# Kernel optimization log

Hardware: AMD Instinct MI355X
Metric: run time of the kernel (lower is better)

## Reference

```python
import jax, jax.numpy as jnp
import numpy as np

HEADS, DK, DV, STRIDE = 8, 32, 32, 2
EPS = 1e-5

def dwconv(x, w, b, stride):
    # depthwise 3x3, padding 1; w: [C,1,3,3]
    y = jax.lax.conv_general_dilated(
        x, w, (stride, stride), ((1, 1), (1, 1)),
        dimension_numbers=("NCHW", "OIHW", "NCHW"),
        feature_group_count=x.shape[1])
    return y + b[None, :, None, None]

def setup_inputs() -> dict:
    key = jax.random.key(0)
    ks = jax.random.split(key, 16)
    B_, C, H, W = 8, 256, 56, 56
    hd = HEADS * DK
    s = lambda k, shp: (jax.random.normal(k, shp, jnp.float32) * 0.02)
    return {
        "x": jax.random.normal(ks[0], (B_, C, H, W), jnp.float32),
        "Wk_dw": s(ks[1], (C, 1, 3, 3)), "bk_dw": jnp.zeros((C,), jnp.float32),
        "Wv_dw": s(ks[2], (C, 1, 3, 3)), "bv_dw": jnp.zeros((C,), jnp.float32),
        "Wq": s(ks[3], (hd, C)), "bq": jnp.zeros((hd,), jnp.float32),
        "Wk": s(ks[4], (hd, C)), "bk": jnp.zeros((hd,), jnp.float32),
        "Wv": s(ks[5], (HEADS * DV, C)), "bv": jnp.zeros((HEADS * DV,), jnp.float32),
        "Wo": s(ks[6], (C, HEADS * DV)), "bo": jnp.zeros((C,), jnp.float32),
        "Bbias": s(ks[7], (1, HEADS, H * W, (H // STRIDE) * (W // STRIDE))),
    }

def reference(x, Wk_dw, bk_dw, Wv_dw, bv_dw, Wq, bq, Wk, bk, Wv, bv, Wo, bo, Bbias):
    b, c, h, w = x.shape
    xr = x.reshape(b, c, h * w).transpose(0, 2, 1)  # [b, hw, c]
    # F.layer_norm with normalized_shape=(b, hw, c): single mean/var over ALL elements
    mu = jnp.mean(xr)
    var = jnp.mean((xr - mu) ** 2)
    xn = (xr - mu) * jax.lax.rsqrt(var + EPS)
    q = (xn @ Wq.T + bq).reshape(b, h * w, HEADS, DK).transpose(0, 2, 1, 3)  # [b,H,hw,dk]
    ki = dwconv(x, Wk_dw, bk_dw, STRIDE)
    kh, kw = ki.shape[2], ki.shape[3]
    kf = ki.reshape(b, c, kh * kw).transpose(0, 2, 1)
    k = (kf @ Wk.T + bk).reshape(b, kh * kw, HEADS, DK).transpose(0, 2, 1, 3)
    vi = dwconv(x, Wv_dw, bv_dw, STRIDE)
    vf = vi.reshape(b, c, kh * kw).transpose(0, 2, 1)
    v = (vf @ Wv.T + bv).reshape(b, kh * kw, HEADS, DV).transpose(0, 2, 1, 3)
    attn = jnp.einsum("bhid,bhjd->bhij", q, k) * (DK ** -0.5) + Bbias
    attn = jax.nn.softmax(attn, axis=-1)
    res = jnp.einsum("bhij,bhjd->bhid", attn, v).transpose(0, 2, 1, 3)
    res = res.reshape(b, h * w, HEADS * DV)
    out = (res @ Wo.T + bo).reshape(b, c, h, w)  # faithful to original .view (no transpose)
    return out + x
```

## Files before the change

### kernel.cpp

```cpp
#include <hip/hip_runtime.h>

typedef unsigned short u16;
typedef unsigned int   u32;
typedef __attribute__((ext_vector_type(8))) short short8;
typedef __attribute__((ext_vector_type(4))) float f32x4;
typedef __attribute__((ext_vector_type(4))) unsigned short us4;

#define MFMA16(a, b, c) __builtin_amdgcn_mfma_f32_16x16x32_bf16((a), (b), (c), 0, 0, 0)

static constexpr int B_ = 8;
static constexpr int HW = 3136;
static constexpr int KW = 784;
static constexpr int NELEM = B_ * 256 * HW;
static constexpr int NBB = 8 * HW * KW;

static constexpr size_t OFF_CNT = 4096;
static constexpr size_t OFF_W   = 8192;
static constexpr int AOFF_WQ = 0, AOFF_WK = 65536, AOFF_WV = 131072, AOFF_WO = 196608;
static constexpr int AOFF_WKDW = 262144, AOFF_WVDW = 264448;
static constexpr int AOFF_BKDW = 266752, AOFF_BVDW = 267008, AOFF_BQ = 267264;
static constexpr int AOFF_BK = 267520, AOFF_BV = 267776, AOFF_BO = 268032;
static constexpr size_t OFF_XT  = 557056;
static constexpr size_t SZ_XT   = (size_t)B_ * HW * 256 * 2;
static constexpr size_t SZ_KJ   = (size_t)B_ * KW * 256 * 2;
static constexpr size_t OFF_KIT = OFF_XT + SZ_XT;
static constexpr size_t OFF_VIT = OFF_KIT + SZ_KJ;
static constexpr size_t OFF_KI  = OFF_VIT + SZ_KJ;
static constexpr size_t OFF_VI  = OFF_KI + SZ_KJ;
static constexpr size_t OFF_Q   = OFF_VI + SZ_KJ;
static constexpr size_t OFF_O   = OFF_XT;
static constexpr size_t OFF_BB  = OFF_Q + SZ_XT;
static constexpr size_t SZ_BB   = (size_t)NBB * 2;

__device__ __forceinline__ float bf2f(u16 u) { return __uint_as_float(((u32)u) << 16); }
__device__ __forceinline__ u16 f2bf(float f) {
  u32 u = __float_as_uint(f);
  u32 r = u + 0x7FFFu + ((u >> 16) & 1u);
  return (u16)(r >> 16);
}
__device__ __forceinline__ u32 cvtpk(float lo, float hi) {
  u32 r;
  asm("v_cvt_pk_bf16_f32 %0, %1, %2" : "=v"(r) : "v"(lo), "v"(hi));
  return r;
}

__global__ __launch_bounds__(256) void detect_k(const u32* __restrict__ x, int* __restrict__ cnt) {
  int c = 0;
  for (int i = threadIdx.x; i < 4096; i += 256) {
    float v = __uint_as_float(x[i] << 16);
    if (fabsf(v) > 1e4f) c++;
  }
#pragma unroll
  for (int off = 32; off > 0; off >>= 1) c += __shfl_down(c, off);
  if ((threadIdx.x & 63) == 0) atomicAdd(cnt, c);
}

struct CvtArgs { const void* src[12]; int dstoff[12]; int n[12]; };
__global__ __launch_bounds__(256) void cvtw_k(CvtArgs a, u16* __restrict__ arena,
                                              const int* __restrict__ cnt) {
  int t = blockIdx.y;
  int n = a.n[t];
  u16* d = arena + a.dstoff[t];
  int f32m = (*cnt >= 64);
  if (f32m) {
    const float* s = (const float*)a.src[t];
    for (int i = blockIdx.x * 256 + threadIdx.x; i < n; i += gridDim.x * 256) d[i] = f2bf(s[i]);
  } else {
    const u16* s = (const u16*)a.src[t];
    for (int i = blockIdx.x * 256 + threadIdx.x; i < n; i += gridDim.x * 256) d[i] = s[i];
  }
}

__global__ __launch_bounds__(256) void cvtb_k(const void* __restrict__ src, u16* __restrict__ dst,
                                              const int* __restrict__ cnt) {
  int f32m = (*cnt >= 64);
  const int n4 = NBB / 4;
  if (f32m) {
    const float4* s = (const float4*)src;
    us4* d = (us4*)dst;
    for (int i = blockIdx.x * 256 + threadIdx.x; i < n4; i += gridDim.x * 256) {
      float4 v = s[i];
      us4 o = {f2bf(v.x), f2bf(v.y), f2bf(v.z), f2bf(v.w)};
      d[i] = o;
    }
  } else {
    const uint2* s = (const uint2*)src;
    uint2* d = (uint2*)dst;
    for (int i = blockIdx.x * 256 + threadIdx.x; i < n4; i += gridDim.x * 256) d[i] = s[i];
  }
}

__global__ __launch_bounds__(256) void reduce_k(const void* __restrict__ x, double* __restrict__ acc,
                                                const int* __restrict__ cnt) {
  int f32m = (*cnt >= 64);
  float s = 0.f, ss = 0.f;
  if (f32m) {
    const float4* xv = (const float4*)x;
    const int n4 = NELEM / 4;
    for (int i = blockIdx.x * 256 + threadIdx.x; i < n4; i += gridDim.x * 256) {
      float4 u = xv[i];
      s += u.x + u.y + u.z + u.w;
      ss += u.x * u.x + u.y * u.y + u.z * u.z + u.w * u.w;
    }
  } else {
    const uint4* xv = (const uint4*)x;
    const int n8 = NELEM / 8;
    for (int i = blockIdx.x * 256 + threadIdx.x; i < n8; i += gridDim.x * 256) {
      uint4 u = xv[i];
      u32 w[4] = {u.x, u.y, u.z, u.w};
#pragma unroll
      for (int q = 0; q < 4; q++) {
        float f0 = __uint_as_float(w[q] << 16);
        float f1 = __uint_as_float(w[q] & 0xFFFF0000u);
        s += f0 + f1;
        ss += f0 * f0 + f1 * f1;
      }
    }
  }
#pragma unroll
  for (int off = 32; off > 0; off >>= 1) {
    s += __shfl_down(s, off);
    ss += __shfl_down(ss, off);
  }
  __shared__ float as_[4], ass_[4];
  int wv = threadIdx.x >> 6;
  if ((threadIdx.x & 63) == 0) { as_[wv] = s; ass_[wv] = ss; }
  __syncthreads();
  if (threadIdx.x == 0) {
    atomicAdd(acc + 0, (double)(as_[0] + as_[1] + as_[2] + as_[3]));
    atomicAdd(acc + 1, (double)(ass_[0] + ass_[1] + ass_[2] + ass_[3]));
  }
}

__global__ __launch_bounds__(256) void prep_k(const u16* __restrict__ wq, const u16* __restrict__ bq,
                                              float* __restrict__ wsf) {
  const double* acc = (const double*)wsf;
  __shared__ float sh[2];
  if (threadIdx.x == 0) {
    double N = (double)NELEM;
    double mu = acc[0] / N;
    double var = acc[1] / N - mu * mu;
    float rstd = (float)(1.0 / sqrt(var + 1e-5));
    sh[0] = (float)mu; sh[1] = rstd;
    wsf[4] = (float)mu; wsf[5] = rstd;
    wsf[6] = rstd * 0.17677669529663687f;
  }
  __syncthreads();
  int o = threadIdx.x;
  float wsum = 0.f;
  for (int c = 0; c < 256; c++) wsum += bf2f(wq[o * 256 + c]);
  wsf[16 + o] = (bf2f(bq[o]) - sh[1] * sh[0] * wsum) * 0.17677669529663687f;
}

__global__ __launch_bounds__(256) void transpose_x_k(const void* __restrict__ src, u16* __restrict__ dst,
                                                     const int* __restrict__ cnt) {
  int f32m = (*cnt >= 64);
  __shared__ u16 t[32][33];
  int b = blockIdx.z;
  int r0 = blockIdx.y * 32, c0 = blockIdx.x * 32;
  int tid = threadIdx.x, col = tid & 31;
  size_t base = (size_t)b * 256 * HW;
  if (f32m) {
    const float* s = (const float*)src + base;
#pragma unroll
    for (int i = 0; i < 4; i++) {
      int row = (tid >> 5) + i * 8;
      t[row][col] = f2bf(s[(size_t)(r0 + row) * HW + c0 + col]);
    }
  } else {
    const u16* s = (const u16*)src + base;
#pragma unroll
    for (int i = 0; i < 4; i++) {
      int row = (tid >> 5) + i * 8;
      t[row][col] = s[(size_t)(r0 + row) * HW + c0 + col];
    }
  }
  __syncthreads();
  u16* d = dst + base;
#pragma unroll
  for (int i = 0; i < 4; i++) {
    int row = (tid >> 5) + i * 8;
    d[(size_t)(c0 + row) * 256 + r0 + col] = t[col][row];
  }
}

__global__ __launch_bounds__(256) void transpose_k(const u16* __restrict__ src, u16* __restrict__ dst,
                                                   int R, int Cc) {
  __shared__ u16 t[32][33];
  int b = blockIdx.z;
  int r0 = blockIdx.y * 32, c0 = blockIdx.x * 32;
  const u16* s = src + (size_t)b * R * Cc;
  u16* d = dst + (size_t)b * R * Cc;
  int tid = threadIdx.x, col = tid & 31;
#pragma unroll
  for (int i = 0; i < 4; i++) {
    int row = (tid >> 5) + i * 8;
    if (r0 + row < R && c0 + col < Cc) t[row][col] = s[(size_t)(r0 + row) * Cc + c0 + col];
  }
  __syncthreads();
#pragma unroll
  for (int i = 0; i < 4; i++) {
    int row = (tid >> 5) + i * 8;
    if (c0 + row < Cc && r0 + col < R) d[(size_t)(c0 + row) * R + r0 + col] = t[col][row];
  }
}

__global__ __launch_bounds__(256) void dwconv_k(const void* __restrict__ x,
                                                const u16* __restrict__ arena,
                                                u16* __restrict__ ki, u16* __restrict__ vi,
                                                const int* __restrict__ cnt) {
  int f32m = (*cnt >= 64);
  int b = blockIdx.x >> 8;
  int c = blockIdx.x & 255;
  float wkf[9], wvf[9];
#pragma unroll
  for (int t = 0; t < 9; t++) {
    wkf[t] = bf2f(arena[AOFF_WKDW + c * 9 + t]);
    wvf[t] = bf2f(arena[AOFF_WVDW + c * 9 + t]);
  }
  float kb = bf2f(arena[AOFF_BKDW + c]), vb = bf2f(arena[AOFF_BVDW + c]);
  size_t xbase = (size_t)(b * 256 + c) * HW;
  auto body = [&](auto LDX) {
    for (int j = threadIdx.x; j < KW; j += 256) {
      int oi = j / 28, oj = j % 28;
      float ka = kb, va = vb;
#pragma unroll
      for (int di = 0; di < 3; di++) {
        int ii = 2 * oi - 1 + di;
        if ((unsigned)ii >= 56u) continue;
#pragma unroll
        for (int dj = 0; dj < 3; dj++) {
          int ij = 2 * oj - 1 + dj;
          if ((unsigned)ij >= 56u) continue;
          float xv = LDX(ii * 56 + ij);
          ka += xv * wkf[di * 3 + dj];
          va += xv * wvf[di * 3 + dj];
        }
      }
      ki[(size_t)(b * 256 + c) * KW + j] = f2bf(ka);
      vi[(size_t)(b * 256 + c) * KW + j] = f2bf(va);
    }
  };
  if (f32m) {
    const float* xp = (const float*)x + xbase;
    body([&](int i) { return xp[i]; });
  } else {
    const u16* xp = (const u16*)x + xbase;
    body([&](int i) { return bf2f(xp[i]); });
  }
}

__global__ __launch_bounds__(256) void proj_q_k(const u16* __restrict__ xt, const u16* __restrict__ Wq,
                                                const float* __restrict__ wsf, u16* __restrict__ q) {
  int lane = threadIdx.x & 63, wave = threadIdx.x >> 6;
  int l15 = lane & 15, quad = lane >> 4;
  int b = blockIdx.x / 49, pb = blockIdx.x % 49;
  int p0 = pb * 64 + wave * 16;
  const u16* arow = xt + ((size_t)(b * HW) + p0 + l15) * 256 + quad * 8;
  short8 af[8];
#pragma unroll
  for (int ks = 0; ks < 8; ks++) af[ks] = *(const short8*)(arow + ks * 32);
  float alpha = wsf[6];
  const float* beta = wsf + 16;
  for (int ot = 0; ot < 16; ot++) {
    const u16* brow = Wq + (size_t)(ot * 16 + l15) * 256 + quad * 8;
    f32x4 acc = {0.f, 0.f, 0.f, 0.f};
#pragma unroll
    for (int ks = 0; ks < 8; ks++) acc = MFMA16(af[ks], *(const short8*)(brow + ks * 32), acc);
    int o = ot * 16 + l15;
    float bet = beta[o];
    size_t base = ((size_t)(b * HW) + p0 + quad * 4) * 256 + o;
#pragma unroll
    for (int r = 0; r < 4; r++) q[base + (size_t)r * 256] = f2bf(alpha * acc[r] + bet);
  }
}

__global__ __launch_bounds__(256) void proj_k_k(const u16* __restrict__ kit, const u16* __restrict__ Wk,
                                                const u16* __restrict__ bk, u16* __restrict__ kout) {
  int lane = threadIdx.x & 63, wave = threadIdx.x >> 6;
  int l15 = lane & 15, quad = lane >> 4;
  int b = blockIdx.x / 13, jb = blockIdx.x % 13;
  int p0 = jb * 64 + wave * 16;
  if (p0 >= KW) return;
  const u16* arow = kit + ((size_t)(b * KW) + p0 + l15) * 256 + quad * 8;
  short8 af[8];
#pragma unroll
  for (int ks = 0; ks < 8; ks++) af[ks] = *(const short8*)(arow + ks * 32);
  for (int ot = 0; ot < 16; ot++) {
    const u16* brow = Wk + (size_t)(ot * 16 + l15) * 256 + quad * 8;
    f32x4 acc = {0.f, 0.f, 0.f, 0.f};
#pragma unroll
    for (int ks = 0; ks < 8; ks++) acc = MFMA16(af[ks], *(const short8*)(brow + ks * 32), acc);
    int o = ot * 16 + l15;
    float bias = bf2f(bk[o]);
    size_t base = ((size_t)(b * KW) + p0 + quad * 4) * 256 + o;
#pragma unroll
    for (int r = 0; r < 4; r++) kout[base + (size_t)r * 256] = f2bf(acc[r] + bias);
  }
}

__global__ __launch_bounds__(256) void proj_v_k(const u16* __restrict__ Wv, const u16* __restrict__ vit,
                                                const u16* __restrict__ bv, u16* __restrict__ vT) {
  int lane = threadIdx.x & 63, wave = threadIdx.x >> 6;
  int l15 = lane & 15, quad = lane >> 4;
  int b = blockIdx.x >> 4;
  int ob = (blockIdx.x >> 2) & 3;
  int js = blockIdx.x & 3;
  int o0 = ob * 64 + wave * 16;
  const u16* arow = Wv + (size_t)(o0 + l15) * 256 + quad * 8;
  short8 af[8];
#pragma unroll
  for (int ks = 0; ks < 8; ks++) af[ks] = *(const short8*)(arow + ks * 32);
  int jt0 = js * 13;
  int jt1 = (jt0 + 13 < 49) ? jt0 + 13 : 49;
  for (int jt = jt0; jt < jt1; jt++) {
    const u16* brow = vit + ((size_t)(b * KW) + jt * 16 + l15) * 256 + quad * 8;
    f32x4 acc = {0.f, 0.f, 0.f, 0.f};
#pragma unroll
    for (int ks = 0; ks < 8; ks++) acc = MFMA16(af[ks], *(const short8*)(brow + ks * 32), acc);
#pragma unroll
    for (int r = 0; r < 4; r++) {
      int o = o0 + quad * 4 + r;
      vT[((size_t)(b * 256) + o) * KW + jt * 16 + l15] = f2bf(acc[r] + bf2f(bv[o]));
    }
  }
}

template <typename LD>
__device__ __forceinline__ void attn_body(const u16* __restrict__ qptr, const u16* __restrict__ kptr,
                                          const u16* __restrict__ vptr, u16* __restrict__ Ob,
                                          int b, int h, int p0, LD ldb) {
  int lane = threadIdx.x & 63;
  int l15 = lane & 15, quad = lane >> 4;
  const u16* qp = qptr + ((size_t)(b * HW) + p0 + l15) * 256 + h * 32 + quad * 8;
  short8 qf0 = *(const short8*)qp;
  short8 qf1 = *(const short8*)(qp + 16 * 256);
  const u16* kb = kptr + (size_t)b * KW * 256 + h * 32 + quad * 8;
  const u16* vb = vptr + ((size_t)(b * 256) + h * 32) * KW;
  const f32x4 zz = {0.f, 0.f, 0.f, 0.f};
  f32x4 o00 = zz, o01 = zz, o10 = zz, o11 = zz;
  float ls0 = 0.f, ls1 = 0.f;
  int sl0 = l15 + ((quad & 1) << 5);
  bool hiq = (quad >= 2);

  auto tile = [&](int jt, u32& q00, u32& q01, u32& q10, u32& q11) {
    short8 kf = *(const short8*)(kb + (size_t)(jt * 16 + l15) * 256);
    f32x4 s0 = MFMA16(kf, qf0, zz);
    f32x4 s1 = MFMA16(kf, qf1, zz);
    f32x4 b0 = ldb(0, jt), b1 = ldb(1, jt);
    float e00 = __expf(fminf(s0[0] + b0[0], 30.f));
    float e01 = __expf(fminf(s0[1] + b0[1], 30.f));
    float e02 = __expf(fminf(s0[2] + b0[2], 30.f));
    float e03 = __expf(fminf(s0[3] + b0[3], 30.f));
    float e10 = __expf(fminf(s1[0] + b1[0], 30.f));
    float e11 = __expf(fminf(s1[1] + b1[1], 30.f));
    float e12 = __expf(fminf(s1[2] + b1[2], 30.f));
    float e13 = __expf(fminf(s1[3] + b1[3], 30.f));
    ls0 += (e00 + e01) + (e02 + e03);
    ls1 += (e10 + e11) + (e12 + e13);
    q00 = cvtpk(e00, e01); q01 = cvtpk(e02, e03);
    q10 = cvtpk(e10, e11); q11 = cvtpk(e12, e13);
  };
  auto gather = [&](u32 pa0, u32 pa1, u32 pb0, u32 pb1) -> short8 {
    u32 a0 = (u32)__shfl((int)pa0, sl0);
    u32 a1 = (u32)__shfl((int)pa1, sl0);
    u32 a2 = (u32)__shfl((int)pa0, sl0 + 16);
    u32 a3 = (u32)__shfl((int)pa1, sl0 + 16);
    u32 c0 = (u32)__shfl((int)pb0, sl0);
    u32 c1 = (u32)__shfl((int)pb1, sl0);
    u32 c2 = (u32)__shfl((int)pb0, sl0 + 16);
    u32 c3 = (u32)__shfl((int)pb1, sl0 + 16);
    union { u32 u[4]; short8 s; } w;
    w.u[0] = hiq ? c0 : a0; w.u[1] = hiq ? c1 : a1;
    w.u[2] = hiq ? c2 : a2; w.u[3] = hiq ? c3 : a3;
    return w.s;
  };
  auto pv = [&](int ch, short8 pf0, short8 pf1) {
    int jo = ch * 32 + quad * 8;
    if (jo > 776) jo = 776;
    short8 v0 = *(const short8*)(vb + (size_t)l15 * KW + jo);
    short8 v1 = *(const short8*)(vb + (size_t)(16 + l15) * KW + jo);
    o00 = MFMA16(pf0, v0, o00); o01 = MFMA16(pf0, v1, o01);
    o10 = MFMA16(pf1, v0, o10); o11 = MFMA16(pf1, v1, o11);
  };

#pragma unroll 2
  for (int ch = 0; ch < 24; ch++) {
    u32 a00, a01, a10, a11, b00, b01, b10, b11;
    tile(ch * 2, a00, a01, a10, a11);
    tile(ch * 2 + 1, b00, b01, b10, b11);
    pv(ch, gather(a00, a01, b00, b01), gather(a10, a11, b10, b11));
  }
  {
    u32 a00, a01, a10, a11;
    tile(48, a00, a01, a10, a11);
    pv(24, gather(a00, a01, 0u, 0u), gather(a10, a11, 0u, 0u));
  }
  ls0 += __shfl_xor(ls0, 16); ls0 += __shfl_xor(ls0, 32);
  ls1 += __shfl_xor(ls1, 16); ls1 += __shfl_xor(ls1, 32);
  float inv0 = 1.f / ls0, inv1 = 1.f / ls1;
  size_t ob0 = ((size_t)(b * HW) + p0 + quad * 4) * 256 + h * 32 + l15;
#pragma unroll
  for (int r = 0; r < 4; r++) {
    float ia = __shfl(inv0, quad * 4 + r);
    float ib = __shfl(inv1, quad * 4 + r);
    Ob[ob0 + (size_t)(r * 256)] = f2bf(o00[r] * ia);
    Ob[ob0 + (size_t)(r * 256) + 16] = f2bf(o01[r] * ia);
    Ob[ob0 + (size_t)(16 * 256 + r * 256)] = f2bf(o10[r] * ib);
    Ob[ob0 + (size_t)(16 * 256 + r * 256) + 16] = f2bf(o11[r] * ib);
  }
}

template <int BMODE>
__global__ __launch_bounds__(64) void attn_k(const u16* __restrict__ q, const u16* __restrict__ k,
                                             const u16* __restrict__ vT, const void* __restrict__ Bb,
                                             u16* __restrict__ Ob, const int* __restrict__ cnt) {
  int lane = threadIdx.x & 63;
  int l15 = lane & 15, quad = lane >> 4;
  int pt = blockIdx.x % 98;
  int t = blockIdx.x / 98;
  int h = t & 7, b = t >> 3;
  int p0 = pt * 32;
  size_t bbase = ((size_t)(h * HW) + p0 + l15) * KW + quad * 4;
  if constexpr (BMODE == 0) {
    const u16* bb = (const u16*)Bb;
    attn_body(q, k, vT, Ob, b, h, p0, [&](int sub, int jt) -> f32x4 {
      us4 v = *(const us4*)(bb + bbase + (size_t)(sub * 16) * KW + jt * 16);
      f32x4 r = {bf2f(v[0]), bf2f(v[1]), bf2f(v[2]), bf2f(v[3])};
      return r;
    });
  } else {
    if (*cnt >= 64) {
      const float* bf = (const float*)Bb;
      attn_body(q, k, vT, Ob, b, h, p0, [&](int sub, int jt) -> f32x4 {
        float4 v = *(const float4*)(bf + bbase + (size_t)(sub * 16) * KW + jt * 16);
        f32x4 r = {v.x, v.y, v.z, v.w};
        return r;
      });
    } else {
      const u16* bb = (const u16*)Bb;
      attn_body(q, k, vT, Ob, b, h, p0, [&](int sub, int jt) -> f32x4 {
        us4 v = *(const us4*)(bb + bbase + (size_t)(sub * 16) * KW + jt * 16);
        f32x4 r = {bf2f(v[0]), bf2f(v[1]), bf2f(v[2]), bf2f(v[3])};
        return r;
      });
    }
  }
}

__global__ __launch_bounds__(256) void proj_o_k(const u16* __restrict__ Ob, const u16* __restrict__ Wo,
                                                const u16* __restrict__ bo, const void* __restrict__ x,
                                                void* __restrict__ out, const int* __restrict__ cnt) {
  int f32m = (*cnt >= 64);
  int lane = threadIdx.x & 63, wave = threadIdx.x >> 6;
  int l15 = lane & 15, quad = lane >> 4;
  int b = blockIdx.x / 49, pb = blockIdx.x % 49;
  int p0 = pb * 64 + wave * 16;
  const u16* arow = Ob + ((size_t)(b * HW) + p0 + l15) * 256 + quad * 8;
  short8 af[8];
#pragma unroll
  for (int ks = 0; ks < 8; ks++) af[ks] = *(const short8*)(arow + ks * 32);
  for (int ot = 0; ot < 16; ot++) {
    const u16* brow = Wo + (size_t)(ot * 16 + l15) * 256 + quad * 8;
    f32x4 acc = {0.f, 0.f, 0.f, 0.f};
#pragma unroll
    for (int ks = 0; ks < 8; ks++) acc = MFMA16(af[ks], *(const short8*)(brow + ks * 32), acc);
    int o = ot * 16 + l15;
    float bias = bf2f(bo[o]);
    if (f32m) {
      const float* xf = (const float*)x;
      float* of = (float*)out;
#pragma unroll
      for (int r = 0; r < 4; r++) {
        size_t idx = ((size_t)(b * HW) + p0 + quad * 4 + r) * 256 + o;
        of[idx] = acc[r] + bias + xf[idx];
      }
    } else {
      const u16* xb = (const u16*)x;
      u16* ob_ = (u16*)out;
#pragma unroll
      for (int r = 0; r < 4; r++) {
        size_t idx = ((size_t)(b * HW) + p0 + quad * 4 + r) * 256 + o;
        ob_[idx] = f2bf(acc[r] + bias + bf2f(xb[idx]));
      }
    }
  }
}

extern "C" void kernel_launch(void* const* d_in, const int* in_sizes, int n_in,
                              void* d_out, int out_size, void* d_ws, size_t ws_size,
                              hipStream_t stream) {
  (void)in_sizes; (void)n_in; (void)out_size;
  const void* x = d_in[0];
  char* ws = (char*)d_ws;
  int* cnt = (int*)(ws + OFF_CNT);
  u16* arena = (u16*)(ws + OFF_W);
  u16* xt  = (u16*)(ws + OFF_XT);
  u16* kit = (u16*)(ws + OFF_KIT);
  u16* vit = (u16*)(ws + OFF_VIT);
  u16* ki  = (u16*)(ws + OFF_KI);
  u16* vi  = (u16*)(ws + OFF_VI);
  u16* qb  = (u16*)(ws + OFF_Q);
  u16* Obuf = (u16*)(ws + OFF_O);
  u16* bbA = (u16*)(ws + OFF_BB);
  bool big_ws = ws_size >= (OFF_BB + SZ_BB);

  CvtArgs a;
  const int srcidx[12] = {5, 7, 9, 11, 1, 3, 2, 4, 6, 8, 10, 12};
  const int dofs[12] = {AOFF_WQ, AOFF_WK, AOFF_WV, AOFF_WO, AOFF_WKDW, AOFF_WVDW,
                        AOFF_BKDW, AOFF_BVDW, AOFF_BQ, AOFF_BK, AOFF_BV, AOFF_BO};
  const int ns[12] = {65536, 65536, 65536, 65536, 2304, 2304, 256, 256, 256, 256, 256, 256};
  for (int i = 0; i < 12; i++) { a.src[i] = d_in[srcidx[i]]; a.dstoff[i] = dofs[i]; a.n[i] = ns[i]; }

  hipMemsetAsync(d_ws, 0, 8192, stream);
  detect_k<<<1, 256, 0, stream>>>((const u32*)x, cnt);
  cvtw_k<<<dim3(32, 12), 256, 0, stream>>>(a, arena, cnt);
  if (big_ws) cvtb_k<<<2048, 256, 0, stream>>>(d_in[13], bbA, cnt);
  reduce_k<<<1024, 256, 0, stream>>>(x, (double*)d_ws, cnt);
  prep_k<<<1, 256, 0, stream>>>(arena + AOFF_WQ, arena + AOFF_BQ, (float*)d_ws);
  transpose_x_k<<<dim3(98, 8, 8), 256, 0, stream>>>(x, xt, cnt);
  dwconv_k<<<2048, 256, 0, stream>>>(x, arena, ki, vi, cnt);
  transpose_k<<<dim3(25, 8, 8), 256, 0, stream>>>(ki, kit, 256, KW);
  transpose_k<<<dim3(25, 8, 8), 256, 0, stream>>>(vi, vit, 256, KW);
  proj_k_k<<<104, 256, 0, stream>>>(kit, arena + AOFF_WK, arena + AOFF_BK, ki);
  proj_v_k<<<128, 256, 0, stream>>>(arena + AOFF_WV, vit, arena + AOFF_BV, vi);
  proj_q_k<<<392, 256, 0, stream>>>(xt, arena + AOFF_WQ, (const float*)d_ws, qb);
  if (big_ws) attn_k<0><<<6272, 64, 0, stream>>>(qb, ki, vi, bbA, Obuf, cnt);
  else        attn_k<1><<<6272, 64, 0, stream>>>(qb, ki, vi, d_in[13], Obuf, cnt);
  proj_o_k<<<392, 256, 0, stream>>>(Obuf, arena + AOFF_WO, arena + AOFF_BO, x, d_out, cnt);
}
```

Baseline: 477.5 us.

## Feed transposed score fragments to PV MFMA per tile and pack four waves per block

Removes the cross-lane shuffle gather that rebuilt the P operand. Each 16-key tile's exponentiated scores now go straight into the PV MFMA as a half-filled (zero-padded) K operand, with V loaded as 4-element chunks. The PV MFMA count doubles and half of each MFMA does no useful work, in exchange for dropping eight shuffles per chunk. Output stores become vectorized 4-element writes, and launches group four 64-thread waves into 256-thread blocks.

```diff
diff --git a/kernel.cpp b/kernel.cpp
--- a/kernel.cpp
+++ b/kernel.cpp
@@ -340,10 +340,8 @@
   const f32x4 zz = {0.f, 0.f, 0.f, 0.f};
   f32x4 o00 = zz, o01 = zz, o10 = zz, o11 = zz;
   float ls0 = 0.f, ls1 = 0.f;
-  int sl0 = l15 + ((quad & 1) << 5);
-  bool hiq = (quad >= 2);
-
-  auto tile = [&](int jt, u32& q00, u32& q01, u32& q10, u32& q11) {
+
+  for (int jt = 0; jt < 49; jt++) {
     short8 kf = *(const short8*)(kb + (size_t)(jt * 16 + l15) * 256);
     f32x4 s0 = MFMA16(kf, qf0, zz);
     f32x4 s1 = MFMA16(kf, qf1, zz);
@@ -358,67 +356,47 @@
     float e13 = __expf(fminf(s1[3] + b1[3], 30.f));
     ls0 += (e00 + e01) + (e02 + e03);
     ls1 += (e10 + e11) + (e12 + e13);
-    q00 = cvtpk(e00, e01); q01 = cvtpk(e02, e03);
-    q10 = cvtpk(e10, e11); q11 = cvtpk(e12, e13);
-  };
-  auto gather = [&](u32 pa0, u32 pa1, u32 pb0, u32 pb1) -> short8 {
-    u32 a0 = (u32)__shfl((int)pa0, sl0);
-    u32 a1 = (u32)__shfl((int)pa1, sl0);
-    u32 a2 = (u32)__shfl((int)pa0, sl0 + 16);
-    u32 a3 = (u32)__shfl((int)pa1, sl0 + 16);
-    u32 c0 = (u32)__shfl((int)pb0, sl0);
-    u32 c1 = (u32)__shfl((int)pb1, sl0);
-    u32 c2 = (u32)__shfl((int)pb0, sl0 + 16);
-    u32 c3 = (u32)__shfl((int)pb1, sl0 + 16);
-    union { u32 u[4]; short8 s; } w;
-    w.u[0] = hiq ? c0 : a0; w.u[1] = hiq ? c1 : a1;
-    w.u[2] = hiq ? c2 : a2; w.u[3] = hiq ? c3 : a3;
-    return w.s;
-  };
-  auto pv = [&](int ch, short8 pf0, short8 pf1) {
-    int jo = ch * 32 + quad * 8;
-    if (jo > 776) jo = 776;
-    short8 v0 = *(const short8*)(vb + (size_t)l15 * KW + jo);
-    short8 v1 = *(const short8*)(vb + (size_t)(16 + l15) * KW + jo);
-    o00 = MFMA16(pf0, v0, o00); o01 = MFMA16(pf0, v1, o01);
-    o10 = MFMA16(pf1, v0, o10); o11 = MFMA16(pf1, v1, o11);
-  };
-
-#pragma unroll 2
-  for (int ch = 0; ch < 24; ch++) {
-    u32 a00, a01, a10, a11, b00, b01, b10, b11;
-    tile(ch * 2, a00, a01, a10, a11);
-    tile(ch * 2 + 1, b00, b01, b10, b11);
-    pv(ch, gather(a00, a01, b00, b01), gather(a10, a11, b10, b11));
-  }
-  {
-    u32 a00, a01, a10, a11;
-    tile(48, a00, a01, a10, a11);
-    pv(24, gather(a00, a01, 0u, 0u), gather(a10, a11, 0u, 0u));
+    union { u32 u[4]; short8 s; } pa, pb;
+    pa.u[0] = cvtpk(e00, e01); pa.u[1] = cvtpk(e02, e03); pa.u[2] = 0; pa.u[3] = 0;
+    pb.u[0] = cvtpk(e10, e11); pb.u[1] = cvtpk(e12, e13); pb.u[2] = 0; pb.u[3] = 0;
+    int jo = jt * 16 + quad * 4;
+    uint2 va2 = *(const uint2*)(vb + (size_t)l15 * KW + jo);
+    uint2 vb2 = *(const uint2*)(vb + (size_t)(16 + l15) * KW + jo);
+    union { u32 u[4]; short8 s; } va, vbf;
+    va.u[0] = va2.x;  va.u[1] = va2.y;  va.u[2] = 0; va.u[3] = 0;
+    vbf.u[0] = vb2.x; vbf.u[1] = vb2.y; vbf.u[2] = 0; vbf.u[3] = 0;
+    o00 = MFMA16(va.s, pa.s, o00);
+    o01 = MFMA16(vbf.s, pa.s, o01);
+    o10 = MFMA16(va.s, pb.s, o10);
+    o11 = MFMA16(vbf.s, pb.s, o11);
   }
   ls0 += __shfl_xor(ls0, 16); ls0 += __shfl_xor(ls0, 32);
   ls1 += __shfl_xor(ls1, 16); ls1 += __shfl_xor(ls1, 32);
   float inv0 = 1.f / ls0, inv1 = 1.f / ls1;
-  size_t ob0 = ((size_t)(b * HW) + p0 + quad * 4) * 256 + h * 32 + l15;
+  size_t ob0 = ((size_t)(b * HW) + p0 + l15) * 256 + h * 32 + quad * 4;
+  us4 w0, w1, w2, w3;
 #pragma unroll
   for (int r = 0; r < 4; r++) {
-    float ia = __shfl(inv0, quad * 4 + r);
-    float ib = __shfl(inv1, quad * 4 + r);
-    Ob[ob0 + (size_t)(r * 256)] = f2bf(o00[r] * ia);
-    Ob[ob0 + (size_t)(r * 256) + 16] = f2bf(o01[r] * ia);
-    Ob[ob0 + (size_t)(16 * 256 + r * 256)] = f2bf(o10[r] * ib);
-    Ob[ob0 + (size_t)(16 * 256 + r * 256) + 16] = f2bf(o11[r] * ib);
-  }
+    w0[r] = f2bf(o00[r] * inv0);
+    w1[r] = f2bf(o01[r] * inv0);
+    w2[r] = f2bf(o10[r] * inv1);
+    w3[r] = f2bf(o11[r] * inv1);
+  }
+  *(us4*)(Ob + ob0) = w0;
+  *(us4*)(Ob + ob0 + 16) = w1;
+  *(us4*)(Ob + ob0 + (size_t)16 * 256) = w2;
+  *(us4*)(Ob + ob0 + (size_t)16 * 256 + 16) = w3;
 }
 
 template <int BMODE>
-__global__ __launch_bounds__(64) void attn_k(const u16* __restrict__ q, const u16* __restrict__ k,
-                                             const u16* __restrict__ vT, const void* __restrict__ Bb,
-                                             u16* __restrict__ Ob, const int* __restrict__ cnt) {
+__global__ __launch_bounds__(256) void attn_k(const u16* __restrict__ q, const u16* __restrict__ k,
+                                              const u16* __restrict__ vT, const void* __restrict__ Bb,
+                                              u16* __restrict__ Ob, const int* __restrict__ cnt) {
   int lane = threadIdx.x & 63;
   int l15 = lane & 15, quad = lane >> 4;
-  int pt = blockIdx.x % 98;
-  int t = blockIdx.x / 98;
+  int task = blockIdx.x * 4 + (threadIdx.x >> 6);
+  int pt = task % 98;
+  int t = task / 98;
   int h = t & 7, b = t >> 3;
   int p0 = pt * 32;
   size_t bbase = ((size_t)(h * HW) + p0 + l15) * KW + quad * 4;
@@ -525,7 +503,7 @@
   proj_k_k<<<104, 256, 0, stream>>>(kit, arena + AOFF_WK, arena + AOFF_BK, ki);
   proj_v_k<<<128, 256, 0, stream>>>(arena + AOFF_WV, vit, arena + AOFF_BV, vi);
   proj_q_k<<<392, 256, 0, stream>>>(xt, arena + AOFF_WQ, (const float*)d_ws, qb);
-  if (big_ws) attn_k<0><<<6272, 64, 0, stream>>>(qb, ki, vi, bbA, Obuf, cnt);
-  else        attn_k<1><<<6272, 64, 0, stream>>>(qb, ki, vi, d_in[13], Obuf, cnt);
+  if (big_ws) attn_k<0><<<1568, 256, 0, stream>>>(qb, ki, vi, bbA, Obuf, cnt);
+  else        attn_k<1><<<1568, 256, 0, stream>>>(qb, ki, vi, d_in[13], Obuf, cnt);
   proj_o_k<<<392, 256, 0, stream>>>(Obuf, arena + AOFF_WO, arena + AOFF_BO, x, d_out, cnt);
 }
```

Result: no change. 479.5 us (+0.4%).
